# Kernel tuning notes

Hardware: AMD Instinct MI355X
Metric: run time of the kernel (lower is better)

The kernel has to match this reference:

```python
import jax, jax.numpy as jnp
import numpy as np

N_NODES = 100000
N_EDGES = 1600000
D_FEAT = 64
K = 5


def setup_inputs() -> dict:
    key = jax.random.key(0)
    k1, k2, k3 = jax.random.split(key, 3)
    feat = jax.random.normal(k1, (N_NODES, D_FEAT), dtype=jnp.float32)
    theta = jnp.asarray([1.0, -0.8, 0.45, -0.2, 0.08], dtype=jnp.float32)
    src = jax.random.randint(k2, (N_EDGES,), 0, N_NODES, dtype=jnp.int32)
    dst = jax.random.randint(k3, (N_EDGES,), 0, N_NODES, dtype=jnp.int32)
    return {"feat": feat, "theta": theta, "src": src, "dst": dst}


def reference(feat, theta, src, dst):
    n = feat.shape[0]
    # in-degrees: number of edges terminating at each node, clamped to >= 1
    deg = jax.ops.segment_sum(jnp.ones_like(dst, dtype=feat.dtype), dst, num_segments=n)
    d_invsqrt = jnp.maximum(deg, 1.0) ** -0.5  # [N]
    d_invsqrt = d_invsqrt[:, None]  # [N, 1]

    def unn_laplacian(x):
        scaled = x * d_invsqrt  # [N, D]
        agg = jax.ops.segment_sum(scaled[src], dst, num_segments=n)  # [N, D]
        return x - agg * d_invsqrt

    h = theta[0] * feat
    for k in range(1, theta.shape[0]):
        feat = unn_laplacian(feat)
        h = h + theta[k] * feat
    return h
```

## Files before the change

kernel.cpp:

```cpp
#include <hip/hip_runtime.h>
#include <hip/hip_bf16.h>
#include <hip/hip_fp16.h>

#define WG 256
#define WGB 1024
#define D 64
#define MAXNB 1024
#define CSRCAP 2048

typedef unsigned long long u64;
typedef unsigned int u32x4 __attribute__((ext_vector_type(4)));
typedef float f32x4 __attribute__((ext_vector_type(4)));

__device__ inline float ld_mixed(const void* p, int bf, long i) {
    if (bf) {
        unsigned short u = ((const unsigned short*)p)[i];
        return __uint_as_float(((unsigned int)u) << 16);
    }
    return ((const float*)p)[i];
}


__global__ __launch_bounds__(WGB) void kc_hist(
        const int* __restrict__ dst, int E, int NBc, int CPB,
        int* __restrict__ histmat,
        const void* __restrict__ theta, int* __restrict__ flag) {
    __shared__ int h[MAXNB];
    int B = blockIdx.x, t = threadIdx.x;
    if (B == 0 && t == 0) {
        unsigned int w = *(const unsigned int*)theta;
        *flag = (w == 0x3F800000u) ? 0 : 1;
    }
    for (int i = t; i < NBc; i += WGB) h[i] = 0;
    __syncthreads();
    int base = B * CPB;
    int end = min(base + CPB, E);
    for (int e = base + t; e < end; e += WGB)
        atomicAdd(&h[dst[e] >> 8], 1);
    __syncthreads();
    for (int i = t; i < NBc; i += WGB)
        histmat[(long)i * NBc + B] = h[i];
}

__global__ void k_scan1(const int* __restrict__ in, int M,
                        int* __restrict__ out, int* __restrict__ part) {
    __shared__ int s[WG];
    int g = blockIdx.x * WG + threadIdx.x;
    int t = threadIdx.x;
    int v0 = (g < M) ? in[g] : 0;
    s[t] = v0;
    __syncthreads();
    for (int o = 1; o < WG; o <<= 1) {
        int v = (t >= o) ? s[t - o] : 0;
        __syncthreads();
        s[t] += v;
        __syncthreads();
    }
    if (g < M) out[g] = s[t] - v0;
    if (t == WG - 1) part[blockIdx.x] = s[t];
}

__global__ __launch_bounds__(WGB) void kc_scatter(
        const int* __restrict__ src, const int* __restrict__ dst, int E,
        int NBc, int CPB, const int* __restrict__ outx,
        const int* __restrict__ part, int P,
        unsigned int* __restrict__ tmp) {
    __shared__ int off[MAXNB];
    __shared__ int ps[1024];
    __shared__ int pex[1024];
    int B = blockIdx.x, t = threadIdx.x;
    int pv = (t < P) ? part[t] : 0;
    ps[t] = pv;
    __syncthreads();
    for (int o = 1; o < 1024; o <<= 1) {
        int v = (t >= o) ? ps[t - o] : 0;
        __syncthreads();
        ps[t] += v;
        __syncthreads();
    }
    pex[t] = ps[t] - pv;
    __syncthreads();
    for (int i = t; i < NBc; i += WGB) {
        long g = (long)i * NBc + B;
        off[i] = outx[g] + pex[g >> 8];
    }
    __syncthreads();
    int base = B * CPB;
    int end = min(base + CPB, E);
    for (int e = base + t; e < end; e += WGB) {
        int d = dst[e];
        int pos = atomicAdd(&off[d >> 8], 1);
        tmp[pos] = (unsigned)src[e] | ((unsigned)(d & 255) << 24);
    }
}

__global__ __launch_bounds__(WGB) void kf(
        const unsigned int* __restrict__ tmp, const int* __restrict__ outx,
        const int* __restrict__ part, int P,
        int NBc, int N, int E, int* __restrict__ ptr,
        float* __restrict__ dinv, float* __restrict__ dsqrt,
        int* __restrict__ csr) {
    __shared__ int h[256];
    __shared__ int pfx[256];
    __shared__ int cnt[256];
    __shared__ int ps[1024];
    __shared__ int pex[1024];
    int B = blockIdx.x, t = threadIdx.x;
    int pv = (t < P) ? part[t] : 0;
    ps[t] = pv;
    __syncthreads();
    for (int o = 1; o < 1024; o <<= 1) {
        int v = (t >= o) ? ps[t - o] : 0;
        __syncthreads();
        ps[t] += v;
        __syncthreads();
    }
    pex[t] = ps[t] - pv;
    __syncthreads();
    long g1 = (long)B * NBc;
    int rbase = outx[g1] + pex[g1 >> 8];
    int rend;
    if (B == NBc - 1) rend = E;
    else {
        long g2 = (long)(B + 1) * NBc;
        rend = outx[g2] + pex[g2 >> 8];
    }
    if (t < 256) h[t] = 0;
    __syncthreads();
    for (int e = rbase + t; e < rend; e += WGB)
        atomicAdd(&h[tmp[e] >> 24], 1);
    __syncthreads();
    if (t < 256) pfx[t] = h[t];
    __syncthreads();
    for (int o = 1; o < 256; o <<= 1) {
        int v = 0;
        if (t < 256 && t >= o) v = pfx[t - o];
        __syncthreads();
        if (t < 256) pfx[t] += v;
        __syncthreads();
    }
    if (t < 256) {
        int ex = pfx[t] - h[t];
        int node = B * 256 + t;
        if (node < N) {
            ptr[node] = rbase + ex;
            float d = (float)h[t];
            d = d < 1.f ? 1.f : d;
            dinv[node]  = rsqrtf(d);
            dsqrt[node] = sqrtf(d);
        }
        cnt[t] = rbase + ex;
    }
    if (B == 0 && t == 0) ptr[N] = E;
    __syncthreads();
    for (int e = rbase + t; e < rend; e += WGB) {
        unsigned p = tmp[e];
        int pos = atomicAdd(&cnt[p >> 24], 1);
        csr[pos] = (int)(p & 0xFFFFFF);
    }
}


__global__ void k_init(const void* __restrict__ feat,
                       const int* __restrict__ flag, const float* __restrict__ dinv,
                       long NF, __half* __restrict__ xs) {
    int bf = *flag;
    long g = ((long)blockIdx.x * WG + threadIdx.x) * 8;
    if (g < NF) {
        float w = dinv[g >> 6];
        float f[8];
#pragma unroll
        for (int j = 0; j < 8; ++j) f[j] = ld_mixed(feat, bf, g + j);
        __half2 a0 = __floats2half2_rn(f[0] * w, f[1] * w);
        __half2 a1 = __floats2half2_rn(f[2] * w, f[3] * w);
        __half2 a2 = __floats2half2_rn(f[4] * w, f[5] * w);
        __half2 a3 = __floats2half2_rn(f[6] * w, f[7] * w);
        u32x4 xo;
        xo.x = *(const unsigned*)&a0; xo.y = *(const unsigned*)&a1;
        xo.z = *(const unsigned*)&a2; xo.w = *(const unsigned*)&a3;
        ((u32x4*)xs)[g >> 3] = xo;
    }
}

#define SPMV_LOOPS(FETCH)                                                  \
    for (; e + 8 <= s1; e += 8) {                                          \
        int idx[8];                                                        \
        _Pragma("unroll")                                                  \
        for (int j = 0; j < 8; ++j) idx[j] = FETCH(e + j);                 \
        uint2 a[8];                                                        \
        _Pragma("unroll")                                                  \
        for (int j = 0; j < 8; ++j) a[j] = xs4[idx[j] * 16 + l];           \
        _Pragma("unroll")                                                  \
        for (int j = 0; j < 8; ++j) {                                      \
            float2 f0 = __half22float2(*(const __half2*)&a[j].x);          \
            float2 f1 = __half22float2(*(const __half2*)&a[j].y);          \
            ax += f0.x; ay += f0.y; az += f1.x; aw += f1.y;                \
        }                                                                  \
    }                                                                      \
    if (e + 4 <= s1) {                                                     \
        int idx[4];                                                        \
        _Pragma("unroll")                                                  \
        for (int j = 0; j < 4; ++j) idx[j] = FETCH(e + j);                 \
        uint2 a[4];                                                        \
        _Pragma("unroll")                                                  \
        for (int j = 0; j < 4; ++j) a[j] = xs4[idx[j] * 16 + l];           \
        _Pragma("unroll")                                                  \
        for (int j = 0; j < 4; ++j) {                                      \
            float2 f0 = __half22float2(*(const __half2*)&a[j].x);          \
            float2 f1 = __half22float2(*(const __half2*)&a[j].y);          \
            ax += f0.x; ay += f0.y; az += f1.x; aw += f1.y;                \
        }                                                                  \
        e += 4;                                                            \
    }                                                                      \
    for (; e < s1; ++e) {                                                  \
        uint2 av = xs4[FETCH(e) * 16 + l];                                 \
        float2 f0 = __half22float2(*(const __half2*)&av.x);                \
        float2 f1 = __half22float2(*(const __half2*)&av.y);                \
        ax += f0.x; ay += f0.y; az += f1.x; aw += f1.y;                    \
    }

#define FETCH_L(x) lcs[(x) - rb]
#define FETCH_G(x) csr[x]

__global__ __launch_bounds__(WG) void k_spmv(
        const __half* __restrict__ xsin,
        const float* __restrict__ dinv, const float* __restrict__ dsqrt,
        const int* __restrict__ ptr, const int* __restrict__ csr,
        const void* __restrict__ theta, const int* __restrict__ flag, int k,
        int N, __half* __restrict__ xsout,
        const __half* __restrict__ xs0, const __half* __restrict__ xs1,
        const __half* __restrict__ xs2,
        void* __restrict__ out, int last) {
    __shared__ int lcs[CSRCAP];
    int t = threadIdx.x;
    int nodeBase = blockIdx.x * 16;
    int lane = t & 63;
    int node = nodeBase + 4 * (t >> 6) + (lane >> 4);
    int l    = lane & 15;

    int nbEnd = min(nodeBase + 16, N);
    int rb = ptr[nodeBase];
    int re = ptr[nbEnd];
    int cntb = re - rb;
    bool useL = (cntb <= CSRCAP);
    if (useL) {
        for (int i = t; i < cntb; i += WG) lcs[i] = csr[rb + i];
    }
    __syncthreads();

    bool valid = node < N;
    int nc = valid ? node : 0;
    int s0 = ptr[nc];
    int s1 = valid ? ptr[nc + 1] : s0;

    const uint2* xs4 = (const uint2*)xsin;
    float ax = 0.f, ay = 0.f, az = 0.f, aw = 0.f;
    int e = s0;
    if (useL) {
        SPMV_LOOPS(FETCH_L)
    } else {
        SPMV_LOOPS(FETCH_G)
    }

    if (!valid) return;
    int o = node * 16 + l;
    float w  = dinv[node];
    float ds = dsqrt[node];
    uint2 xv = xs4[o];
    float2 x0 = __half22float2(*(const __half2*)&xv.x);
    float2 x1 = __half22float2(*(const __half2*)&xv.y);
    float u0 = x0.x * ds, u1 = x0.y * ds, u2 = x1.x * ds, u3 = x1.y * ds;
    float v0 = u0 - w * ax;
    float v1 = u1 - w * ay;
    float v2 = u2 - w * az;
    float v3 = u3 - w * aw;
    if (!last) {
        __half2 t0 = __floats2half2_rn(v0 * w, v1 * w);
        __half2 t1 = __floats2half2_rn(v2 * w, v3 * w);
        uint2 xo;
        xo.x = *(const unsigned*)&t0; xo.y = *(const unsigned*)&t1;
        ((uint2*)xsout)[o] = xo;
        return;
    }
    int bf = *flag;
    float th0 = ld_mixed(theta, bf, 0);
    float th1 = ld_mixed(theta, bf, 1);
    float th2 = ld_mixed(theta, bf, 2);
    float th3 = ld_mixed(theta, bf, 3);
    float th4 = ld_mixed(theta, bf, 4);
    uint2 r0 = ((const uint2*)xs0)[o];
    uint2 r1 = ((const uint2*)xs1)[o];
    uint2 r2 = ((const uint2*)xs2)[o];
    float2 a0 = __half22float2(*(const __half2*)&r0.x);
    float2 a1 = __half22float2(*(const __half2*)&r0.y);
    float2 b0 = __half22float2(*(const __half2*)&r1.x);
    float2 b1 = __half22float2(*(const __half2*)&r1.y);
    float2 c0 = __half22float2(*(const __half2*)&r2.x);
    float2 c1 = __half22float2(*(const __half2*)&r2.y);
    float h0 = th0 * a0.x * ds + th1 * b0.x * ds + th2 * c0.x * ds + th3 * u0 + th4 * v0;
    float h1 = th0 * a0.y * ds + th1 * b0.y * ds + th2 * c0.y * ds + th3 * u1 + th4 * v1;
    float h2 = th0 * a1.x * ds + th1 * b1.x * ds + th2 * c1.x * ds + th3 * u2 + th4 * v2;
    float h3 = th0 * a1.y * ds + th1 * b1.y * ds + th2 * c1.y * ds + th3 * u3 + th4 * v3;
    if (bf) {
        __hip_bfloat162 q0, q1;
        q0.x = __float2bfloat16(h0); q0.y = __float2bfloat16(h1);
        q1.x = __float2bfloat16(h2); q1.y = __float2bfloat16(h3);
        u64 r = (u64)(*(const unsigned*)&q0) |
                ((u64)(*(const unsigned*)&q1) << 32);
        __builtin_nontemporal_store(r, (u64*)out + o);
    } else {
        f32x4 r; r.x = h0; r.y = h1; r.z = h2; r.w = h3;
        __builtin_nontemporal_store(r, (f32x4*)out + o);
    }
}

extern "C" void kernel_launch(void* const* d_in, const int* in_sizes, int n_in,
                              void* d_out, int out_size, void* d_ws, size_t ws_size,
                              hipStream_t stream) {
    const void* feat  = d_in[0];
    const void* theta = d_in[1];
    const int*  src   = (const int*)d_in[2];
    const int*  dst   = (const int*)d_in[3];
    long NF = in_sizes[0];
    int  N  = (int)(NF / D);
    int  E  = in_sizes[2];

    int NBc = (N + 255) >> 8;
    int CPB = (E + NBc - 1) / NBc;
    int M   = NBc * NBc;
    int sbl = (M + WG - 1) / WG;

    char* w = (char*)d_ws;
    size_t off = 0;
    auto alloc = [&](size_t b) -> void* {
        void* p = w + off;
        off = (off + b + 255) & ~(size_t)255;
        return p;
    };
    int*      histmat = (int*)alloc((size_t)M * 4);
    int*      outx    = (int*)alloc((size_t)M * 4);
    int*      part    = (int*)alloc(1024 * 4);
    unsigned* tmp     = (unsigned*)alloc((size_t)E * 4);
    int*      ptr     = (int*)alloc(((size_t)N + 1) * 4);
    int*      csr     = (int*)alloc((size_t)E * 4);
    float*    dinv    = (float*)alloc((size_t)N * 4);
    float*    dsqrt   = (float*)alloc((size_t)N * 4);
    int*      flag    = (int*)alloc(4);
    __half*   xs0     = (__half*)alloc((size_t)NF * 2);
    __half*   xs1     = (__half*)alloc((size_t)NF * 2);
    __half*   xs2     = (__half*)alloc((size_t)NF * 2);
    __half*   xs3     = (__half*)alloc((size_t)NF * 2);

    int fbl = (int)((NF / 8 + WG - 1) / WG);
    int wbl = (N + 15) / 16;

    kc_hist<<<NBc, WGB, 0, stream>>>(dst, E, NBc, CPB, histmat, theta, flag);
    k_scan1<<<sbl, WG, 0, stream>>>(histmat, M, outx, part);
    kc_scatter<<<NBc, WGB, 0, stream>>>(src, dst, E, NBc, CPB, outx, part, sbl, tmp);
    kf<<<NBc, WGB, 0, stream>>>(tmp, outx, part, sbl, NBc, N, E, ptr, dinv, dsqrt, csr);
    k_init<<<fbl, WG, 0, stream>>>(feat, flag, dinv, NF, xs0);

    __half* chain[5] = { xs0, xs1, xs2, xs3, nullptr };
    for (int k = 1; k <= 4; ++k) {
        int last = (k == 4);
        k_spmv<<<wbl, WG, 0, stream>>>(chain[k - 1], dinv, dsqrt, ptr, csr,
                                       theta, flag, k, N, chain[k],
                                       xs0, xs1, xs2, d_out, last);
    }
}
```

Baseline: 255.7 us.

## Stage CSR build scatter through LDS buckets to coalesce global writes

In kc_scatter, each block first sorts its edges into coarse destination buckets in shared memory, using a local prefix scan of its histogram column. It then writes them out to tmp in contiguous runs instead of as scattered global writes. kf likewise places edges into a shared buffer before writing csr sequentially whenever the bucket span fits in KFCAP. The aim is to cut uncoalesced scattered stores during CSR construction, at the cost of more LDS per block (dynamic CPB*8 bytes plus 24KB in kf), which may lower occupancy. The SPMV macro is also reworked with no change in behaviour.

```diff
diff --git a/kernel.cpp b/kernel.cpp
--- a/kernel.cpp
+++ b/kernel.cpp
@@ -7,6 +7,7 @@
 #define D 64
 #define MAXNB 1024
 #define CSRCAP 2048
+#define KFCAP 6144
 
 typedef unsigned long long u64;
 typedef unsigned int u32x4 __attribute__((ext_vector_type(4)));
@@ -64,10 +65,15 @@
         const int* __restrict__ src, const int* __restrict__ dst, int E,
         int NBc, int CPB, const int* __restrict__ outx,
         const int* __restrict__ part, int P,
+        const int* __restrict__ histmat,
         unsigned int* __restrict__ tmp) {
     __shared__ int off[MAXNB];
+    __shared__ int lh[MAXNB];
     __shared__ int ps[1024];
     __shared__ int pex[1024];
+    extern __shared__ unsigned sb[];
+    unsigned* sbv = sb;
+    int* sbp = (int*)(sb + CPB);
     int B = blockIdx.x, t = threadIdx.x;
     int pv = (t < P) ? part[t] : 0;
     ps[t] = pv;
@@ -80,18 +86,40 @@
     }
     pex[t] = ps[t] - pv;
     __syncthreads();
-    for (int i = t; i < NBc; i += WGB) {
-        long g = (long)i * NBc + B;
-        off[i] = outx[g] + pex[g >> 8];
+    if (t < NBc) {
+        long g = (long)t * NBc + B;
+        off[t] = outx[g] + pex[g >> 8];
+        lh[t]  = histmat[(long)t * NBc + B];
+    }
+    __syncthreads();
+    int v0 = (t < NBc) ? lh[t] : 0;
+    ps[t] = v0;
+    __syncthreads();
+    for (int o = 1; o < 1024; o <<= 1) {
+        int v = (t >= o) ? ps[t - o] : 0;
+        __syncthreads();
+        ps[t] += v;
+        __syncthreads();
+    }
+    if (t < NBc) {
+        int ex = ps[t] - v0;
+        lh[t] = ex;
+        off[t] -= ex;
     }
     __syncthreads();
     int base = B * CPB;
     int end = min(base + CPB, E);
+    int nE = end - base;
     for (int e = base + t; e < end; e += WGB) {
         int d = dst[e];
-        int pos = atomicAdd(&off[d >> 8], 1);
-        tmp[pos] = (unsigned)src[e] | ((unsigned)(d & 255) << 24);
-    }
+        int q = d >> 8;
+        int li = atomicAdd(&lh[q], 1);
+        sbv[li] = (unsigned)src[e] | ((unsigned)(d & 255) << 24);
+        sbp[li] = off[q] + li;
+    }
+    __syncthreads();
+    for (int li = t; li < nE; li += WGB)
+        tmp[sbp[li]] = sbv[li];
 }
 
 __global__ __launch_bounds__(WGB) void kf(
@@ -105,6 +133,7 @@
     __shared__ int cnt[256];
     __shared__ int ps[1024];
     __shared__ int pex[1024];
+    __shared__ unsigned sbuf[KFCAP];
     int B = blockIdx.x, t = threadIdx.x;
     int pv = (t < P) ? part[t] : 0;
     ps[t] = pv;
@@ -139,6 +168,8 @@
         if (t < 256) pfx[t] += v;
         __syncthreads();
     }
+    int span = rend - rbase;
+    bool useS = (span <= KFCAP);
     if (t < 256) {
         int ex = pfx[t] - h[t];
         int node = B * 256 + t;
@@ -149,14 +180,25 @@
             dinv[node]  = rsqrtf(d);
             dsqrt[node] = sqrtf(d);
         }
-        cnt[t] = rbase + ex;
+        cnt[t] = useS ? ex : (rbase + ex);
     }
     if (B == 0 && t == 0) ptr[N] = E;
     __syncthreads();
-    for (int e = rbase + t; e < rend; e += WGB) {
-        unsigned p = tmp[e];
-        int pos = atomicAdd(&cnt[p >> 24], 1);
-        csr[pos] = (int)(p & 0xFFFFFF);
+    if (useS) {
+        for (int e = rbase + t; e < rend; e += WGB) {
+            unsigned p = tmp[e];
+            int pos = atomicAdd(&cnt[p >> 24], 1);
+            sbuf[pos] = p & 0xFFFFFFu;
+        }
+        __syncthreads();
+        for (int i = t; i < span; i += WGB)
+            csr[rbase + i] = (int)sbuf[i];
+    } else {
+        for (int e = rbase + t; e < rend; e += WGB) {
+            unsigned p = tmp[e];
+            int pos = atomicAdd(&cnt[p >> 24], 1);
+            csr[pos] = (int)(p & 0xFFFFFF);
+        }
     }
 }
 
@@ -182,45 +224,31 @@
     }
 }
 
-#define SPMV_LOOPS(FETCH)                                                  \
-    for (; e + 8 <= s1; e += 8) {                                          \
-        int idx[8];                                                        \
+#define SPMV_CHUNK(NN)                                                     \
+    {                                                                      \
+        int idx[NN];                                                       \
         _Pragma("unroll")                                                  \
-        for (int j = 0; j < 8; ++j) idx[j] = FETCH(e + j);                 \
-        uint2 a[8];                                                        \
+        for (int j = 0; j < NN; ++j) idx[j] = FETCH(e + j);                \
+        uint2 a[NN];                                                       \
         _Pragma("unroll")                                                  \
-        for (int j = 0; j < 8; ++j) a[j] = xs4[idx[j] * 16 + l];           \
+        for (int j = 0; j < NN; ++j) a[j] = xs4[idx[j] * 16 + l];          \
         _Pragma("unroll")                                                  \
-        for (int j = 0; j < 8; ++j) {                                      \
+        for (int j = 0; j < NN; ++j) {                                     \
             float2 f0 = __half22float2(*(const __half2*)&a[j].x);          \
             float2 f1 = __half22float2(*(const __half2*)&a[j].y);          \
             ax += f0.x; ay += f0.y; az += f1.x; aw += f1.y;                \
         }                                                                  \
-    }                                                                      \
-    if (e + 4 <= s1) {                                                     \
-        int idx[4];                                                        \
-        _Pragma("unroll")                                                  \
-        for (int j = 0; j < 4; ++j) idx[j] = FETCH(e + j);                 \
-        uint2 a[4];                                                        \
-        _Pragma("unroll")                                                  \
-        for (int j = 0; j < 4; ++j) a[j] = xs4[idx[j] * 16 + l];           \
-        _Pragma("unroll")                                                  \
-        for (int j = 0; j < 4; ++j) {                                      \
-            float2 f0 = __half22float2(*(const __half2*)&a[j].x);          \
-            float2 f1 = __half22float2(*(const __half2*)&a[j].y);          \
-            ax += f0.x; ay += f0.y; az += f1.x; aw += f1.y;                \
-        }                                                                  \
-        e += 4;                                                            \
-    }                                                                      \
+    }
+
+#define SPMV_LOOPS                                                         \
+    for (; e + 8 <= s1; e += 8) SPMV_CHUNK(8)                              \
+    if (e + 4 <= s1) { SPMV_CHUNK(4) e += 4; }                             \
     for (; e < s1; ++e) {                                                  \
         uint2 av = xs4[FETCH(e) * 16 + l];                                 \
         float2 f0 = __half22float2(*(const __half2*)&av.x);                \
         float2 f1 = __half22float2(*(const __half2*)&av.y);                \
         ax += f0.x; ay += f0.y; az += f1.x; aw += f1.y;                    \
     }
-
-#define FETCH_L(x) lcs[(x) - rb]
-#define FETCH_G(x) csr[x]
 
 __global__ __launch_bounds__(WG) void k_spmv(
         const __half* __restrict__ xsin,
@@ -257,9 +285,13 @@
     float ax = 0.f, ay = 0.f, az = 0.f, aw = 0.f;
     int e = s0;
     if (useL) {
-        SPMV_LOOPS(FETCH_L)
+#define FETCH(x) lcs[(x) - rb]
+        SPMV_LOOPS
+#undef FETCH
     } else {
-        SPMV_LOOPS(FETCH_G)
+#define FETCH(x) csr[x]
+        SPMV_LOOPS
+#undef FETCH
     }
 
     if (!valid) return;
@@ -353,10 +385,12 @@
 
     int fbl = (int)((NF / 8 + WG - 1) / WG);
     int wbl = (N + 15) / 16;
+    size_t dynls = (size_t)CPB * 8;
 
     kc_hist<<<NBc, WGB, 0, stream>>>(dst, E, NBc, CPB, histmat, theta, flag);
     k_scan1<<<sbl, WG, 0, stream>>>(histmat, M, outx, part);
-    kc_scatter<<<NBc, WGB, 0, stream>>>(src, dst, E, NBc, CPB, outx, part, sbl, tmp);
+    kc_scatter<<<NBc, WGB, dynls, stream>>>(src, dst, E, NBc, CPB, outx, part,
+                                            sbl, histmat, tmp);
     kf<<<NBc, WGB, 0, stream>>>(tmp, outx, part, sbl, NBc, N, E, ptr, dinv, dsqrt, csr);
     k_init<<<fbl, WG, 0, stream>>>(feat, flag, dinv, NF, xs0);
 
```

After: 251.0 us. About the same (-1.8%).
